# Kernel tuning notes

Hardware: AMD Instinct MI355X
Metric: run time of the kernel (lower is better)

## Reference

```python
import jax, jax.numpy as jnp
import numpy as np

B, NQ, NK, H = 4, 256, 512, 256

def setup_inputs() -> dict:
    key = jax.random.key(0)
    k1, k2, k3, k4, k5 = jax.random.split(key, 5)
    s = 1.0 / np.sqrt(H)
    return {
        "x_query": jax.random.normal(k1, (B, NQ, H), dtype=jnp.float32),
        "x_key": jax.random.normal(k2, (B, NK, H), dtype=jnp.float32),
        "w1": jax.random.uniform(k3, (H, H), jnp.float32, -s, s),  # torch Linear weight (out,in)
        "w2": jax.random.uniform(k4, (H, H), jnp.float32, -s, s),
        "v": jax.random.uniform(k5, (1, H), jnp.float32, -s, s),
    }

def reference(x_query, x_key, w1, w2, v):
    # key_transform: (B, NK, H); query_transform: (B, NQ, H)
    kt = jnp.einsum('bkh,oh->bko', x_key, w1)
    qt = jnp.einsum('bqh,oh->bqo', x_query, w2)
    # broadcast add -> (B, NQ, NK, H), tanh, project with v -> (B, NQ, NK)
    prod = jnp.einsum('bqkh,h->bqk', jnp.tanh(kt[:, None, :, :] + qt[:, :, None, :]), v[0])
    return jax.nn.log_softmax(prod, axis=-1)
```

## Files before the change

kernel.cpp:

```cpp
#include <hip/hip_runtime.h>

#define B_  4
#define NQ_ 256
#define NK_ 512
#define H_  256
#define PADK 520

typedef _Float16 half8  __attribute__((ext_vector_type(8)));
typedef _Float16 half4_t __attribute__((ext_vector_type(4)));

#define TWO_LOG2E 2.8853900817779268f

__global__ __launch_bounds__(256)
void gemm_fused(const float* __restrict__ xq, const float* __restrict__ xk,
                const float* __restrict__ w1, const float* __restrict__ w2,
                _Float16* __restrict__ Ebuf,
                float* __restrict__ Fbuf)
{
    constexpr int BK = 32;
    const float* A; const float* Bm;
    int m0, n0, bz; bool iskt;
    {
        int id = blockIdx.x;
        if (id < 128) {
            iskt = true;
            bz = id >> 5; int t = id & 31;
            m0 = (t >> 3) * 64; n0 = (t & 7) * 64;
            A = w1; Bm = xk + (long)bz * NK_ * H_;
        } else {
            iskt = false;
            id -= 128;
            bz = id >> 4; int t = id & 15;
            m0 = (t >> 2) * 64; n0 = (t & 3) * 64;
            A = xq + (long)bz * NQ_ * H_; Bm = w2;
        }
    }
    const int lda = H_, ldb = H_;
    const int ks = (blockIdx.x & 7) * BK;

    __shared__ float As[BK][68];
    __shared__ float Bs[BK][68];

    const int tid  = threadIdx.x;
    const int lrow = tid >> 2;
    const int lk   = (tid & 3) * 8;
    const int tm   = (tid >> 4) * 4;
    const int tn   = (tid & 15) * 4;

    float acc[4][4] = {};

    float4 a0_r = *(const float4*)&A [(long)(m0 + lrow) * lda + ks + lk];
    float4 a1_r = *(const float4*)&A [(long)(m0 + lrow) * lda + ks + lk + 4];
    float4 b0_r = *(const float4*)&Bm[(long)(n0 + lrow) * ldb + ks + lk];
    float4 b1_r = *(const float4*)&Bm[(long)(n0 + lrow) * ldb + ks + lk + 4];
    float4 a0_n = a0_r, a1_n = a1_r, b0_n = b0_r, b1_n = b1_r;

    for (int t = 0; t < H_; t += BK) {
        __syncthreads();
        As[lk+0][lrow]=a0_r.x; As[lk+1][lrow]=a0_r.y; As[lk+2][lrow]=a0_r.z; As[lk+3][lrow]=a0_r.w;
        As[lk+4][lrow]=a1_r.x; As[lk+5][lrow]=a1_r.y; As[lk+6][lrow]=a1_r.z; As[lk+7][lrow]=a1_r.w;
        Bs[lk+0][lrow]=b0_r.x; Bs[lk+1][lrow]=b0_r.y; Bs[lk+2][lrow]=b0_r.z; Bs[lk+3][lrow]=b0_r.w;
        Bs[lk+4][lrow]=b1_r.x; Bs[lk+5][lrow]=b1_r.y; Bs[lk+6][lrow]=b1_r.z; Bs[lk+7][lrow]=b1_r.w;
        if (t + BK < H_) {
            const int ktn = (ks + t + BK) & (H_ - 1);
            a0_n = *(const float4*)&A [(long)(m0 + lrow) * lda + ktn + lk];
            a1_n = *(const float4*)&A [(long)(m0 + lrow) * lda + ktn + lk + 4];
            b0_n = *(const float4*)&Bm[(long)(n0 + lrow) * ldb + ktn + lk];
            b1_n = *(const float4*)&Bm[(long)(n0 + lrow) * ldb + ktn + lk + 4];
        }
        __syncthreads();
        #pragma unroll
        for (int kk = 0; kk < BK; ++kk) {
            float4 av = *(const float4*)&As[kk][tm];
            float4 bv = *(const float4*)&Bs[kk][tn];
            float am[4] = {av.x, av.y, av.z, av.w};
            float bn[4] = {bv.x, bv.y, bv.z, bv.w};
            #pragma unroll
            for (int i = 0; i < 4; ++i)
                #pragma unroll
                for (int j = 0; j < 4; ++j)
                    acc[i][j] = fmaf(am[i], bn[j], acc[i][j]);
        }
        a0_r = a0_n; a1_r = a1_n; b0_r = b0_n; b1_r = b1_n;
    }

    if (iskt) {
        const long gbase = ((long)bz * 32 + ((m0 + tm) >> 3)) * PADK * 8 + (tm & 7);
        #pragma unroll
        for (int j = 0; j < 4; ++j) {
            half4_t h4;
            #pragma unroll
            for (int i = 0; i < 4; ++i) {
                float e = __builtin_amdgcn_exp2f(acc[i][j] * TWO_LOG2E);
                h4[i] = (_Float16)fminf(e, 60000.0f);
            }
            *(half4_t*)&Ebuf[gbase + (long)(n0 + tn + j) * 8] = h4;
        }
    } else {
        #pragma unroll
        for (int i = 0; i < 4; ++i) {
            float4 f4v = { __builtin_amdgcn_exp2f(acc[i][0] * TWO_LOG2E),
                           __builtin_amdgcn_exp2f(acc[i][1] * TWO_LOG2E),
                           __builtin_amdgcn_exp2f(acc[i][2] * TWO_LOG2E),
                           __builtin_amdgcn_exp2f(acc[i][3] * TWO_LOG2E) };
            *(float4*)&Fbuf[((long)bz * NQ_ + m0 + tm + i) * H_ + n0 + tn] = f4v;
        }
    }
}

__global__ __launch_bounds__(512, 2)
void attn_main(const half8* __restrict__ Eh,
               const float* __restrict__ Fbuf,
               const float* __restrict__ v,
               float* __restrict__ out)
{
    const int k = threadIdx.x, b = blockIdx.y, q0 = blockIdx.x * 2;
    const int sb = (blockIdx.x & 7) * 4;

    const half8* kp   = Eh + (long)b * 32 * PADK + k;
    const float4* F0p = (const float4*)(Fbuf + ((long)b * NQ_ + q0) * H_);
    const float4* F1p = F0p + (H_ / 4);
    const float4* v4p = (const float4*)v;

    float T0 = 0.f, T1 = 0.f;

    half8 ka0 = kp[(long)(sb + 0) * PADK], ka1 = kp[(long)(sb + 1) * PADK],
          ka2 = kp[(long)(sb + 2) * PADK], ka3 = kp[(long)(sb + 3) * PADK];
    half8 kn0 = ka0, kn1 = ka1, kn2 = ka2, kn3 = ka3;

#define QTERM(T, E0, E1, E2, E3, FQ, VV)                                      \
    {                                                                         \
        float d0 = fmaf(E0, FQ.x, 1.f), d1 = fmaf(E1, FQ.y, 1.f);             \
        float d2 = fmaf(E2, FQ.z, 1.f), d3 = fmaf(E3, FQ.w, 1.f);             \
        float D01 = d0 * d1, D23 = d2 * d3;                                   \
        float N01 = fmaf(VV.x, d1, VV.y * d0);                                \
        float N23 = fmaf(VV.z, d3, VV.w * d2);                                \
        float N   = fmaf(N01, D23, N23 * D01);                                \
        T = fmaf(N, __builtin_amdgcn_rcpf(D01 * D23), T);                     \
    }
#define PROW(KV, R)                                                           \
    {                                                                         \
        float e0 = (float)KV[0], e1 = (float)KV[1], e2 = (float)KV[2],        \
              e3 = (float)KV[3], e4 = (float)KV[4], e5 = (float)KV[5],        \
              e6 = (float)KV[6], e7 = (float)KV[7];                           \
        float4 va  = v4p[2*(R)],   vb  = v4p[2*(R)+1];                        \
        float4 f0a = F0p[2*(R)],   f0b = F0p[2*(R)+1];                        \
        float4 f1a = F1p[2*(R)],   f1b = F1p[2*(R)+1];                        \
        QTERM(T0, e0, e1, e2, e3, f0a, va)                                    \
        QTERM(T0, e4, e5, e6, e7, f0b, vb)                                    \
        QTERM(T1, e0, e1, e2, e3, f1a, va)                                    \
        QTERM(T1, e4, e5, e6, e7, f1b, vb)                                    \
    }

    for (int gg = 0; gg < 32; gg += 4) {
        const int g = (gg + sb) & 31;
        if (gg + 4 < 32) {
            const int gn = (g + 4) & 31;
            kn0 = kp[(long)(gn + 0) * PADK];
            kn1 = kp[(long)(gn + 1) * PADK];
            kn2 = kp[(long)(gn + 2) * PADK];
            kn3 = kp[(long)(gn + 3) * PADK];
        }
        PROW(ka0, g + 0)
        PROW(ka1, g + 1)
        PROW(ka2, g + 2)
        PROW(ka3, g + 3)
        ka0 = kn0; ka1 = kn1; ka2 = kn2; ka3 = kn3;
    }
#undef PROW
#undef QTERM

    float val0 = -2.f * T0;
    float val1 = -2.f * T1;

    __shared__ float red[8][2];
    const int lane = k & 63, wv = k >> 6;

    float e0 = __builtin_amdgcn_exp2f(val0 * 1.4426950408889634f);
    float e1 = __builtin_amdgcn_exp2f(val1 * 1.4426950408889634f);
    #pragma unroll
    for (int o = 32; o; o >>= 1) {
        e0 += __shfl_xor(e0, o, 64);
        e1 += __shfl_xor(e1, o, 64);
    }
    if (lane == 0) { red[wv][0] = e0; red[wv][1] = e1; }
    __syncthreads();
    float s0 = 0.f, s1 = 0.f;
    #pragma unroll
    for (int w = 0; w < 8; ++w) { s0 += red[w][0]; s1 += red[w][1]; }

    float l0 = __builtin_amdgcn_logf(s0) * 0.6931471805599453f;
    float l1 = __builtin_amdgcn_logf(s1) * 0.6931471805599453f;
    out[((long)b * NQ_ + q0 + 0) * NK_ + k] = val0 - l0;
    out[((long)b * NQ_ + q0 + 1) * NK_ + k] = val1 - l1;
}

extern "C" void kernel_launch(void* const* d_in, const int* in_sizes, int n_in,
                              void* d_out, int out_size, void* d_ws, size_t ws_size,
                              hipStream_t stream)
{
    const float* xq = (const float*)d_in[0];
    const float* xk = (const float*)d_in[1];
    const float* w1 = (const float*)d_in[2];
    const float* w2 = (const float*)d_in[3];
    const float* v  = (const float*)d_in[4];
    float* out = (float*)d_out;

    _Float16* Ebuf = (_Float16*)d_ws;
    float* Fbuf = (float*)((char*)d_ws + (size_t)B_ * 32 * PADK * 8 * 2);

    gemm_fused<<<dim3(192), 256, 0, stream>>>(xq, xk, w1, w2, Ebuf, Fbuf);
    attn_main<<<dim3(NQ_ / 2, B_), 512, 0, stream>>>(
        (const half8*)Ebuf, Fbuf, v, out);
}
```

Measured before the change: 34.49 us.

## Split-K the projection GEMM across two thread groups, process four queries per attention block

```diff
diff --git a/kernel.cpp b/kernel.cpp
--- a/kernel.cpp
+++ b/kernel.cpp
@@ -11,7 +11,7 @@
 
 #define TWO_LOG2E 2.8853900817779268f
 
-__global__ __launch_bounds__(256)
+__global__ __launch_bounds__(512)
 void gemm_fused(const float* __restrict__ xq, const float* __restrict__ xk,
                 const float* __restrict__ w1, const float* __restrict__ w2,
                 _Float16* __restrict__ Ebuf,
@@ -38,10 +38,13 @@
     const int lda = H_, ldb = H_;
     const int ks = (blockIdx.x & 7) * BK;
 
-    __shared__ float As[BK][68];
-    __shared__ float Bs[BK][68];
-
-    const int tid  = threadIdx.x;
+    __shared__ float As[2][BK][68];
+    __shared__ float Bs[2][BK][68];
+    __shared__ float Cred[16][260];
+
+    const int tid  = threadIdx.x & 255;
+    const int grp  = threadIdx.x >> 8;
+    const int kofs = grp * 128;
     const int lrow = tid >> 2;
     const int lk   = (tid & 3) * 8;
     const int tm   = (tid >> 4) * 4;
@@ -49,20 +52,25 @@
 
     float acc[4][4] = {};
 
-    float4 a0_r = *(const float4*)&A [(long)(m0 + lrow) * lda + ks + lk];
-    float4 a1_r = *(const float4*)&A [(long)(m0 + lrow) * lda + ks + lk + 4];
-    float4 b0_r = *(const float4*)&Bm[(long)(n0 + lrow) * ldb + ks + lk];
-    float4 b1_r = *(const float4*)&Bm[(long)(n0 + lrow) * ldb + ks + lk + 4];
+    int kt0 = (ks + kofs) & (H_ - 1);
+    float4 a0_r = *(const float4*)&A [(long)(m0 + lrow) * lda + kt0 + lk];
+    float4 a1_r = *(const float4*)&A [(long)(m0 + lrow) * lda + kt0 + lk + 4];
+    float4 b0_r = *(const float4*)&Bm[(long)(n0 + lrow) * ldb + kt0 + lk];
+    float4 b1_r = *(const float4*)&Bm[(long)(n0 + lrow) * ldb + kt0 + lk + 4];
     float4 a0_n = a0_r, a1_n = a1_r, b0_n = b0_r, b1_n = b1_r;
 
-    for (int t = 0; t < H_; t += BK) {
+    for (int t = 0; t < 128; t += BK) {
         __syncthreads();
-        As[lk+0][lrow]=a0_r.x; As[lk+1][lrow]=a0_r.y; As[lk+2][lrow]=a0_r.z; As[lk+3][lrow]=a0_r.w;
-        As[lk+4][lrow]=a1_r.x; As[lk+5][lrow]=a1_r.y; As[lk+6][lrow]=a1_r.z; As[lk+7][lrow]=a1_r.w;
-        Bs[lk+0][lrow]=b0_r.x; Bs[lk+1][lrow]=b0_r.y; Bs[lk+2][lrow]=b0_r.z; Bs[lk+3][lrow]=b0_r.w;
-        Bs[lk+4][lrow]=b1_r.x; Bs[lk+5][lrow]=b1_r.y; Bs[lk+6][lrow]=b1_r.z; Bs[lk+7][lrow]=b1_r.w;
-        if (t + BK < H_) {
-            const int ktn = (ks + t + BK) & (H_ - 1);
+        As[grp][lk+0][lrow]=a0_r.x; As[grp][lk+1][lrow]=a0_r.y;
+        As[grp][lk+2][lrow]=a0_r.z; As[grp][lk+3][lrow]=a0_r.w;
+        As[grp][lk+4][lrow]=a1_r.x; As[grp][lk+5][lrow]=a1_r.y;
+        As[grp][lk+6][lrow]=a1_r.z; As[grp][lk+7][lrow]=a1_r.w;
+        Bs[grp][lk+0][lrow]=b0_r.x; Bs[grp][lk+1][lrow]=b0_r.y;
+        Bs[grp][lk+2][lrow]=b0_r.z; Bs[grp][lk+3][lrow]=b0_r.w;
+        Bs[grp][lk+4][lrow]=b1_r.x; Bs[grp][lk+5][lrow]=b1_r.y;
+        Bs[grp][lk+6][lrow]=b1_r.z; Bs[grp][lk+7][lrow]=b1_r.w;
+        if (t + BK < 128) {
+            const int ktn = (ks + kofs + t + BK) & (H_ - 1);
             a0_n = *(const float4*)&A [(long)(m0 + lrow) * lda + ktn + lk];
             a1_n = *(const float4*)&A [(long)(m0 + lrow) * lda + ktn + lk + 4];
             b0_n = *(const float4*)&Bm[(long)(n0 + lrow) * ldb + ktn + lk];
@@ -71,8 +79,8 @@
         __syncthreads();
         #pragma unroll
         for (int kk = 0; kk < BK; ++kk) {
-            float4 av = *(const float4*)&As[kk][tm];
-            float4 bv = *(const float4*)&Bs[kk][tn];
+            float4 av = *(const float4*)&As[grp][kk][tm];
+            float4 bv = *(const float4*)&Bs[grp][kk][tn];
             float am[4] = {av.x, av.y, av.z, av.w};
             float bn[4] = {bv.x, bv.y, bv.z, bv.w};
             #pragma unroll
@@ -84,26 +92,43 @@
         a0_r = a0_n; a1_r = a1_n; b0_r = b0_n; b1_r = b1_n;
     }
 
-    if (iskt) {
-        const long gbase = ((long)bz * 32 + ((m0 + tm) >> 3)) * PADK * 8 + (tm & 7);
-        #pragma unroll
-        for (int j = 0; j < 4; ++j) {
-            half4_t h4;
+    __syncthreads();
+    if (grp == 1) {
+        #pragma unroll
+        for (int i = 0; i < 4; ++i)
+            #pragma unroll
+            for (int j = 0; j < 4; ++j)
+                Cred[i * 4 + j][tid] = acc[i][j];
+    }
+    __syncthreads();
+    if (grp == 0) {
+        #pragma unroll
+        for (int i = 0; i < 4; ++i)
+            #pragma unroll
+            for (int j = 0; j < 4; ++j)
+                acc[i][j] += Cred[i * 4 + j][tid];
+
+        if (iskt) {
+            const long gbase = ((long)bz * 32 + ((m0 + tm) >> 3)) * PADK * 8 + (tm & 7);
+            #pragma unroll
+            for (int j = 0; j < 4; ++j) {
+                half4_t h4;
+                #pragma unroll
+                for (int i = 0; i < 4; ++i) {
+                    float e = __builtin_amdgcn_exp2f(acc[i][j] * TWO_LOG2E);
+                    h4[i] = (_Float16)fminf(e, 60000.0f);
+                }
+                *(half4_t*)&Ebuf[gbase + (long)(n0 + tn + j) * 8] = h4;
+            }
+        } else {
             #pragma unroll
             for (int i = 0; i < 4; ++i) {
-                float e = __builtin_amdgcn_exp2f(acc[i][j] * TWO_LOG2E);
-                h4[i] = (_Float16)fminf(e, 60000.0f);
+                float4 f4v = { __builtin_amdgcn_exp2f(acc[i][0] * TWO_LOG2E),
+                               __builtin_amdgcn_exp2f(acc[i][1] * TWO_LOG2E),
+                               __builtin_amdgcn_exp2f(acc[i][2] * TWO_LOG2E),
+                               __builtin_amdgcn_exp2f(acc[i][3] * TWO_LOG2E) };
+                *(float4*)&Fbuf[((long)bz * NQ_ + m0 + tm + i) * H_ + n0 + tn] = f4v;
             }
-            *(half4_t*)&Ebuf[gbase + (long)(n0 + tn + j) * 8] = h4;
-        }
-    } else {
-        #pragma unroll
-        for (int i = 0; i < 4; ++i) {
-            float4 f4v = { __builtin_amdgcn_exp2f(acc[i][0] * TWO_LOG2E),
-                           __builtin_amdgcn_exp2f(acc[i][1] * TWO_LOG2E),
-                           __builtin_amdgcn_exp2f(acc[i][2] * TWO_LOG2E),
-                           __builtin_amdgcn_exp2f(acc[i][3] * TWO_LOG2E) };
-            *(float4*)&Fbuf[((long)bz * NQ_ + m0 + tm + i) * H_ + n0 + tn] = f4v;
         }
     }
 }
@@ -114,15 +139,17 @@
                const float* __restrict__ v,
                float* __restrict__ out)
 {
-    const int k = threadIdx.x, b = blockIdx.y, q0 = blockIdx.x * 2;
+    const int k = threadIdx.x, b = blockIdx.y, q0 = blockIdx.x * 4;
     const int sb = (blockIdx.x & 7) * 4;
 
     const half8* kp   = Eh + (long)b * 32 * PADK + k;
     const float4* F0p = (const float4*)(Fbuf + ((long)b * NQ_ + q0) * H_);
     const float4* F1p = F0p + (H_ / 4);
+    const float4* F2p = F1p + (H_ / 4);
+    const float4* F3p = F2p + (H_ / 4);
     const float4* v4p = (const float4*)v;
 
-    float T0 = 0.f, T1 = 0.f;
+    float T0 = 0.f, T1 = 0.f, T2 = 0.f, T3 = 0.f;
 
     half8 ka0 = kp[(long)(sb + 0) * PADK], ka1 = kp[(long)(sb + 1) * PADK],
           ka2 = kp[(long)(sb + 2) * PADK], ka3 = kp[(long)(sb + 3) * PADK];
@@ -145,11 +172,17 @@
               e6 = (float)KV[6], e7 = (float)KV[7];                           \
         float4 va  = v4p[2*(R)],   vb  = v4p[2*(R)+1];                        \
         float4 f0a = F0p[2*(R)],   f0b = F0p[2*(R)+1];                        \
-        float4 f1a = F1p[2*(R)],   f1b = F1p[2*(R)+1];                        \
         QTERM(T0, e0, e1, e2, e3, f0a, va)                                    \
         QTERM(T0, e4, e5, e6, e7, f0b, vb)                                    \
+        float4 f1a = F1p[2*(R)],   f1b = F1p[2*(R)+1];                        \
         QTERM(T1, e0, e1, e2, e3, f1a, va)                                    \
         QTERM(T1, e4, e5, e6, e7, f1b, vb)                                    \
+        float4 f2a = F2p[2*(R)],   f2b = F2p[2*(R)+1];                        \
+        QTERM(T2, e0, e1, e2, e3, f2a, va)                                    \
+        QTERM(T2, e4, e5, e6, e7, f2b, vb)                                    \
+        float4 f3a = F3p[2*(R)],   f3b = F3p[2*(R)+1];                        \
+        QTERM(T3, e0, e1, e2, e3, f3a, va)                                    \
+        QTERM(T3, e4, e5, e6, e7, f3b, vb)                                    \
     }
 
     for (int gg = 0; gg < 32; gg += 4) {
@@ -170,29 +203,27 @@
 #undef PROW
 #undef QTERM
 
-    float val0 = -2.f * T0;
-    float val1 = -2.f * T1;
-
-    __shared__ float red[8][2];
+    float val[4] = { -2.f * T0, -2.f * T1, -2.f * T2, -2.f * T3 };
+
+    __shared__ float red[8][4];
     const int lane = k & 63, wv = k >> 6;
 
-    float e0 = __builtin_amdgcn_exp2f(val0 * 1.4426950408889634f);
-    float e1 = __builtin_amdgcn_exp2f(val1 * 1.4426950408889634f);
     #pragma unroll
-    for (int o = 32; o; o >>= 1) {
-        e0 += __shfl_xor(e0, o, 64);
-        e1 += __shfl_xor(e1, o, 64);
-    }
-    if (lane == 0) { red[wv][0] = e0; red[wv][1] = e1; }
+    for (int j = 0; j < 4; ++j) {
+        float e = __builtin_amdgcn_exp2f(val[j] * 1.4426950408889634f);
+        #pragma unroll
+        for (int o = 32; o; o >>= 1) e += __shfl_xor(e, o, 64);
+        if (lane == 0) red[wv][j] = e;
+    }
     __syncthreads();
-    float s0 = 0.f, s1 = 0.f;
     #pragma unroll
-    for (int w = 0; w < 8; ++w) { s0 += red[w][0]; s1 += red[w][1]; }
-
-    float l0 = __builtin_amdgcn_logf(s0) * 0.6931471805599453f;
-    float l1 = __builtin_amdgcn_logf(s1) * 0.6931471805599453f;
-    out[((long)b * NQ_ + q0 + 0) * NK_ + k] = val0 - l0;
-    out[((long)b * NQ_ + q0 + 1) * NK_ + k] = val1 - l1;
+    for (int j = 0; j < 4; ++j) {
+        float s = 0.f;
+        #pragma unroll
+        for (int w = 0; w < 8; ++w) s += red[w][j];
+        float l = __builtin_amdgcn_logf(s) * 0.6931471805599453f;
+        out[((long)b * NQ_ + q0 + j) * NK_ + k] = val[j] - l;
+    }
 }
 
 extern "C" void kernel_launch(void* const* d_in, const int* in_sizes, int n_in,
@@ -209,7 +240,7 @@
     _Float16* Ebuf = (_Float16*)d_ws;
     float* Fbuf = (float*)((char*)d_ws + (size_t)B_ * 32 * PADK * 8 * 2);
 
-    gemm_fused<<<dim3(192), 256, 0, stream>>>(xq, xk, w1, w2, Ebuf, Fbuf);
-    attn_main<<<dim3(NQ_ / 2, B_), 512, 0, stream>>>(
+    gemm_fused<<<dim3(192), 512, 0, stream>>>(xq, xk, w1, w2, Ebuf, Fbuf);
+    attn_main<<<dim3(NQ_ / 4, B_), 512, 0, stream>>>(
         (const half8*)Ebuf, Fbuf, v, out);
 }
```

After: 34.61 us. No clear change (+0.4%).
